# Kernel tuning notes

Hardware: AMD Instinct MI355X
Metric: run time of the kernel (lower is better)

The kernel has to match this reference:

```python
import jax, jax.numpy as jnp
import numpy as np

NUM_HEADS = 16
HEAD_DIM = 64  # d_out // num_heads


def setup_inputs() -> dict:
    key = jax.random.key(0)
    ks = jax.random.split(key, 6)
    d_in, d_out, b, t = 1024, 1024, 2, 2048
    s = 0.02
    return {
        "x": jax.random.normal(ks[0], (b, t, d_in), jnp.float32),
        "Wq": jax.random.normal(ks[1], (d_in, d_out), jnp.float32) * s,
        "Wk": jax.random.normal(ks[2], (d_in, d_out), jnp.float32) * s,
        "Wv": jax.random.normal(ks[3], (d_in, d_out), jnp.float32) * s,
        "Wo": jax.random.normal(ks[4], (d_out, d_out), jnp.float32) * s,
        "bo": jnp.zeros((d_out,), jnp.float32),
    }


def reference(x, Wq, Wk, Wv, Wo, bo):
    b, t, _ = x.shape
    H, hd = NUM_HEADS, HEAD_DIM
    # qkv projections (no bias), split into heads: [b, H, t, hd]
    q = (x @ Wq).reshape(b, t, H, hd).transpose(0, 2, 1, 3)
    k = (x @ Wk).reshape(b, t, H, hd).transpose(0, 2, 1, 3)
    v = (x @ Wv).reshape(b, t, H, hd).transpose(0, 2, 1, 3)
    # raw scores, causal mask (masked_fill with -1e9 BEFORE the 1/sqrt(hd) scale,
    # matching the source exactly), then scaled softmax
    scores = jnp.einsum("bhqd,bhkd->bhqk", q, k)
    causal = jnp.triu(jnp.ones((t, t), dtype=bool), k=1)
    scores = jnp.where(causal[None, None], jnp.float32(-1e9), scores)
    attn = jax.nn.softmax(scores / jnp.sqrt(jnp.float32(hd)), axis=-1)
    # dropout is identity in eval mode
    ctx = jnp.einsum("bhqk,bhkd->bhqd", attn, v)  # [b, H, t, hd]
    ctx = ctx.transpose(0, 2, 1, 3).reshape(b, t, H * hd)
    return ctx @ Wo + bo
```

## Files before the change

kernel.cpp:

```cpp
#include <hip/hip_runtime.h>


#define SEQ   2048
#define DMODEL 1024
#define NH    16
#define HD    64
#define MROWS 4096

typedef __attribute__((ext_vector_type(4))) float f32x4;
typedef __attribute__((ext_vector_type(16))) float f32x16;
typedef __attribute__((ext_vector_type(8))) short short8;
typedef __attribute__((ext_vector_type(4))) unsigned int u32x4;

#define MFMA16(a, b, c) __builtin_amdgcn_mfma_f32_16x16x32_bf16((a), (b), (c), 0, 0, 0)
#define MFMA32(a, b, c) __builtin_amdgcn_mfma_f32_32x32x16_bf16((a), (b), (c), 0, 0, 0)

__device__ __forceinline__ unsigned short f2bf(float f) {
  union { float f; unsigned u; } v; v.f = f;
  return (unsigned short)((v.u + 0x7fffu + ((v.u >> 16) & 1u)) >> 16);
}

__device__ __forceinline__ float exp2x(float x) {
#if __has_builtin(__builtin_amdgcn_exp2f)
  return __builtin_amdgcn_exp2f(x);
#else
  float r; asm("v_exp_f32 %0, %1" : "=v"(r) : "v"(x)); return r;
#endif
}

__device__ __forceinline__ unsigned cvt_pk(float lo, float hi) {
  unsigned r;
  asm volatile("v_cvt_pk_bf16_f32 %0, %1, %2" : "=v"(r) : "v"(lo), "v"(hi));
  return r;
}

__device__ __forceinline__ void pls(unsigned& a, unsigned& b) {
  asm("v_permlane32_swap_b32 %0, %1" : "+v"(a), "+v"(b));
}

__device__ __forceinline__ short8 as_short8(u32x4 v) {
  union { u32x4 u; short8 s; } x; x.u = v; return x.s;
}

__device__ __forceinline__ f32x4 zero4() {
  f32x4 z; z[0] = 0.f; z[1] = 0.f; z[2] = 0.f; z[3] = 0.f; return z;
}

__device__ __forceinline__ void async16(const void* g, void* l) {
  __builtin_amdgcn_global_load_lds(
      (const __attribute__((address_space(1))) unsigned int*)g,
      (__attribute__((address_space(3))) unsigned int*)l, 16, 0, 0);
}

__global__ __launch_bounds__(256) void xconv(const float* __restrict__ x,
                                             unsigned short* __restrict__ xb) {
  int i = blockIdx.x * 256 + threadIdx.x;
  const float4* p = (const float4*)x;
  float4 a = p[2 * i];
  float4 b = p[2 * i + 1];
  short8 o;
  o[0] = (short)f2bf(a.x); o[1] = (short)f2bf(a.y);
  o[2] = (short)f2bf(a.z); o[3] = (short)f2bf(a.w);
  o[4] = (short)f2bf(b.x); o[5] = (short)f2bf(b.y);
  o[6] = (short)f2bf(b.z); o[7] = (short)f2bf(b.w);
  *(short8*)&xb[(size_t)i * 8] = o;
}

__global__ __launch_bounds__(256) void wtrans(const float* __restrict__ W,
                                              unsigned short* __restrict__ Wt) {
  __shared__ unsigned short tile[64][65];
  int t = threadIdx.x;
  int tx = t & 63, ty = t >> 6;
  int kb = blockIdx.x * 64, nb = blockIdx.y * 64;
#pragma unroll
  for (int rr = 0; rr < 16; rr++) {
    int r = ty * 16 + rr;
    tile[r][tx] = f2bf(W[(size_t)(kb + r) * 1024 + nb + tx]);
  }
  __syncthreads();
#pragma unroll
  for (int rr = 0; rr < 16; rr++) {
    int r = ty * 16 + rr;
    Wt[(size_t)(nb + r) * 1024 + kb + tx] = tile[tx][r];
  }
}

__global__ __launch_bounds__(256) void vtrans(const unsigned short* __restrict__ V,
                                              unsigned short* __restrict__ Vt) {
  __shared__ unsigned short tile[64][65];
  int t = threadIdx.x;
  int tx = t & 63, ty = t >> 6;
  int bh = blockIdx.x, t0 = blockIdx.y * 64;
  const unsigned short* src = V + ((size_t)bh * SEQ + t0) * HD;
  unsigned short* dst = Vt + (size_t)bh * HD * SEQ + t0;
#pragma unroll
  for (int rr = 0; rr < 16; rr++) {
    int r = ty * 16 + rr;
    tile[r][tx] = src[(size_t)r * HD + tx];
  }
  __syncthreads();
#pragma unroll
  for (int rr = 0; rr < 16; rr++) {
    int r = ty * 16 + rr;
    dst[(size_t)r * SEQ + tx] = tile[tx][r];
  }
}

template <int MODE, int WMF>
__global__ __launch_bounds__(256) void gemm_bt(
    const unsigned short* __restrict__ A, const unsigned short* __restrict__ Bt,
    unsigned short* __restrict__ Qo, unsigned short* __restrict__ Ko,
    unsigned short* __restrict__ Vo, float* __restrict__ out,
    const float* __restrict__ bo) {
  constexpr int K = 1024;
  constexpr int BM = WMF * 32;
  constexpr int NT = K / 32;
  __shared__ __align__(16) unsigned short As[3][BM * 32];
  __shared__ __align__(16) unsigned short Bs[3][128 * 32];
  const int t = threadIdx.x;
  const int lane = t & 63;
  const int w = t >> 6;
  const int lr = lane & 15, kf = lane >> 4;
  const int wr = w >> 1, wc = w & 1;

  const int nwg = gridDim.x * gridDim.y;
  const int id = blockIdx.y * gridDim.x + blockIdx.x;
  const int swz = (id & 7) * (nwg >> 3) + (id >> 3);
  const int bx = swz % gridDim.x, by = swz / gridDim.x;

  const int rowbase = bx * BM;
  const int colbase = by * 128;

  const unsigned short* Ab = A + (size_t)rowbase * K;
  const unsigned short* Bb = Bt + (size_t)colbase * K;

  f32x4 acc[WMF][4];
#pragma unroll
  for (int m = 0; m < WMF; m++)
#pragma unroll
    for (int n = 0; n < 4; n++) acc[m][n] = zero4();

  auto stage = [&](int buf, int kt) {
    int k0 = kt * 32;
#pragma unroll
    for (int i = 0; i < BM / 64; i++) {
      int f = i * 256 + t;
      int c = f ^ ((f >> 3) & 3);
      int row = c >> 2;
      int col = (c & 3) << 3;
      async16(Ab + (size_t)row * K + k0 + col, (char*)&As[buf][0] + (size_t)f * 16);
    }
#pragma unroll
    for (int i = 0; i < 2; i++) {
      int f = i * 256 + t;
      int c = f ^ ((f >> 3) & 3);
      int row = c >> 2;
      int col = (c & 3) << 3;
      async16(Bb + (size_t)row * K + k0 + col, (char*)&Bs[buf][0] + (size_t)f * 16);
    }
  };

  stage(0, 0);
  stage(1, 1);

  for (int kt = 0; kt < NT; kt++) {
    if (kt + 2 < NT) {
      stage((kt + 2) % 3, kt + 2);
      if constexpr (MODE == 0) asm volatile("s_waitcnt vmcnt(8)" ::: "memory");
      else                     asm volatile("s_waitcnt vmcnt(6)" ::: "memory");
    } else if (kt + 1 < NT) {
      if constexpr (MODE == 0) asm volatile("s_waitcnt vmcnt(4)" ::: "memory");
      else                     asm volatile("s_waitcnt vmcnt(3)" ::: "memory");
    } else {
      asm volatile("s_waitcnt vmcnt(0)" ::: "memory");
    }
    __builtin_amdgcn_s_barrier();

    const int cur = kt % 3;
    short8 av[WMF], bv[4];
#pragma unroll
    for (int m = 0; m < WMF; m++) {
      int row = wr * (WMF * 16) + m * 16 + lr;
      int idx = (row * 32 + kf * 8) ^ (((row >> 1) & 3) << 3);
      av[m] = *(const short8*)&As[cur][idx];
    }
#pragma unroll
    for (int n = 0; n < 4; n++) {
      int row = wc * 64 + n * 16 + lr;
      int idx = (row * 32 + kf * 8) ^ (((row >> 1) & 3) << 3);
      bv[n] = *(const short8*)&Bs[cur][idx];
    }
    __builtin_amdgcn_s_setprio(1);
#pragma unroll
    for (int m = 0; m < WMF; m++)
#pragma unroll
      for (int n = 0; n < 4; n++) acc[m][n] = MFMA16(av[m], bv[n], acc[m][n]);
    __builtin_amdgcn_s_setprio(0);
    __builtin_amdgcn_s_barrier();
  }

  if constexpr (MODE == 0) {
#pragma unroll
    for (int n = 0; n < 4; n++) {
      int c = colbase + wc * 64 + n * 16 + lr;
      int sel = c >> 10;
      int hh = (c >> 6) & 15;
      int dd = c & 63;
      unsigned short* dst = (sel == 0) ? Qo : ((sel == 1) ? Ko : Vo);
      const float sc = (sel == 0) ? 0.18033688011112042f : 1.0f;
#pragma unroll
      for (int m = 0; m < WMF; m++) {
        int r0 = rowbase + wr * (WMF * 16) + m * 16 + kf * 4;
#pragma unroll
        for (int i = 0; i < 4; i++) {
          int r = r0 + i;
          int bi = r >> 11;
          int tq = r & 2047;
          size_t off = ((size_t)(bi * NH + hh) * SEQ + tq) * HD + dd;
          dst[off] = f2bf(acc[m][n][i] * sc);
        }
      }
    }
  } else {
#pragma unroll
    for (int n = 0; n < 4; n++) {
      int c = colbase + wc * 64 + n * 16 + lr;
      float bias = bo[c];
#pragma unroll
      for (int m = 0; m < WMF; m++) {
        int r0 = rowbase + wr * (WMF * 16) + m * 16 + kf * 4;
#pragma unroll
        for (int i = 0; i < 4; i++) {
          out[(size_t)(r0 + i) * 1024 + c] = acc[m][n][i] + bias;
        }
      }
    }
  }
}

__global__ __launch_bounds__(256) void attn_fwd(
    const unsigned short* __restrict__ Q, const unsigned short* __restrict__ K,
    const unsigned short* __restrict__ Vt, unsigned short* __restrict__ ctx) {
  const int bh = blockIdx.x;
  const int y = blockIdx.y;
  const int qt = (y < 8) ? (15 - y) : (y - 8);
  const int bi = bh >> 4, hh = bh & 15;
  const int t = threadIdx.x, lane = t & 63, w = t >> 6;
  const int qc = lane & 31, hi = lane >> 5;

  __shared__ __align__(16) unsigned short Ks[2][2][64 * 64];
  __shared__ __align__(16) unsigned short Vs[2][2][64 * 64];

  const unsigned short* Qb = Q + (size_t)bh * SEQ * HD;
  const unsigned short* Kb = K + (size_t)bh * SEQ * HD;
  const unsigned short* Vb = Vt + (size_t)bh * HD * SEQ;

  const int qrow = qt * 128 + w * 32;
  short8 qv[4];
#pragma unroll
  for (int c = 0; c < 4; c++)
    qv[c] = *(const short8*)&Qb[(size_t)(qrow + qc) * HD + c * 16 + hi * 8];

  f32x16 o0, o1;
#pragma unroll
  for (int i = 0; i < 16; i++) { o0[i] = 0.f; o1[i] = 0.f; }
  float l_acc = 0.f;

  const int ktmax = 2 * qt + (w >> 1);
  const int NP = qt + 1;

  auto stage = [&](int buf, int p) {
#pragma unroll
    for (int sub = 0; sub < 2; sub++) {
      int kt = 2 * p + sub;
#pragma unroll
      for (int i2 = 0; i2 < 2; i2++) {
        int f = i2 * 256 + t;
        int c = f ^ ((f >> 3) & 7);
        async16(Kb + (size_t)kt * 64 * HD + (size_t)c * 8,
                (char*)&Ks[buf][sub][0] + (size_t)f * 16);
        int d = c >> 3, ko = (c & 7) << 3;
        async16(Vb + (size_t)d * SEQ + (size_t)kt * 64 + ko,
                (char*)&Vs[buf][sub][0] + (size_t)f * 16);
      }
    }
  };

  auto tile = [&](const unsigned short* Kt, const unsigned short* Vtile, int kt) {
    f32x16 s0, s1;
#pragma unroll
    for (int i = 0; i < 16; i++) { s0[i] = 0.f; s1[i] = 0.f; }
    __builtin_amdgcn_s_setprio(1);
#pragma unroll
    for (int c = 0; c < 4; c++) {
      int i0 = (qc * 64 + c * 16 + hi * 8) ^ ((qc & 7) << 3);
      s0 = MFMA32(*(const short8*)&Kt[i0], qv[c], s0);
      int r1 = 32 + qc;
      int i1 = (r1 * 64 + c * 16 + hi * 8) ^ ((r1 & 7) << 3);
      s1 = MFMA32(*(const short8*)&Kt[i1], qv[c], s1);
    }
    __builtin_amdgcn_s_setprio(0);

    if (kt == ktmax) {
      const int qg = qrow + qc;
#pragma unroll
      for (int reg = 0; reg < 16; reg++) {
        int rloc = (reg & 3) + 8 * (reg >> 2) + 4 * hi;
        int kg = kt * 64 + rloc;
        if (kg > qg) s0[reg] = -1e30f;
        if (kg + 32 > qg) s1[reg] = -1e30f;
      }
    }

    unsigned w0[8], w1[8];
    float psA = 0.f, psB = 0.f;
#pragma unroll
    for (int j = 0; j < 8; j++) {
      float a0 = exp2x(s0[2 * j]), b0 = exp2x(s0[2 * j + 1]);
      float a1 = exp2x(s1[2 * j]), b1 = exp2x(s1[2 * j + 1]);
      psA += a0 + b0;
      psB += a1 + b1;
      w0[j] = cvt_pk(a0, b0);
      w1[j] = cvt_pk(a1, b1);
    }
    l_acc += psA + psB;

    __builtin_amdgcn_s_setprio(1);
#pragma unroll
    for (int h2 = 0; h2 < 2; h2++) {
      unsigned* pw = h2 ? w1 : w0;
#pragma unroll
      for (int cc = 0; cc < 2; cc++) {
        unsigned a0 = pw[cc * 4 + 0], b0 = pw[cc * 4 + 2];
        unsigned a1 = pw[cc * 4 + 1], b1 = pw[cc * 4 + 3];
        pls(a0, b0);
        pls(a1, b1);
        u32x4 pf; pf[0] = a0; pf[1] = a1; pf[2] = b0; pf[3] = b1;
        short8 pfrag = as_short8(pf);
        int c2 = h2 * 2 + cc;
        int ia = (qc * 64 + c2 * 16 + hi * 8) ^ ((qc & 7) << 3);
        o0 = MFMA32(*(const short8*)&Vtile[ia], pfrag, o0);
        int rb = 32 + qc;
        int ib = (rb * 64 + c2 * 16 + hi * 8) ^ ((rb & 7) << 3);
        o1 = MFMA32(*(const short8*)&Vtile[ib], pfrag, o1);
      }
    }
    __builtin_amdgcn_s_setprio(0);
  };

  stage(0, 0);
  int cur = 0;

  for (int p = 0; p < NP; p++) {
    if (p + 1 < NP) {
      stage(cur ^ 1, p + 1);
      asm volatile("s_waitcnt vmcnt(8)" ::: "memory");
    } else {
      asm volatile("s_waitcnt vmcnt(0)" ::: "memory");
    }
    __builtin_amdgcn_s_barrier();

    if (2 * p <= ktmax)     tile(&Ks[cur][0][0], &Vs[cur][0][0], 2 * p);
    if (2 * p + 1 <= ktmax) tile(&Ks[cur][1][0], &Vs[cur][1][0], 2 * p + 1);

    __builtin_amdgcn_s_barrier();
    cur ^= 1;
  }

  float l = l_acc + __shfl_xor(l_acc, 32);
  float inv = 1.0f / l;
  const size_t rowoff = ((size_t)bi * SEQ + qrow + qc) * DMODEL + hh * HD;
#pragma unroll
  for (int g = 0; g < 4; g++) {
    unsigned pa = cvt_pk(o0[4 * g] * inv, o0[4 * g + 1] * inv);
    unsigned pb = cvt_pk(o0[4 * g + 2] * inv, o0[4 * g + 3] * inv);
    uint2 vv; vv.x = pa; vv.y = pb;
    *(uint2*)&ctx[rowoff + 8 * g + 4 * hi] = vv;
    unsigned pc = cvt_pk(o1[4 * g] * inv, o1[4 * g + 1] * inv);
    unsigned pd = cvt_pk(o1[4 * g + 2] * inv, o1[4 * g + 3] * inv);
    uint2 ww; ww.x = pc; ww.y = pd;
    *(uint2*)&ctx[rowoff + 32 + 8 * g + 4 * hi] = ww;
  }
}

extern "C" void kernel_launch(void* const* d_in, const int* in_sizes, int n_in,
                              void* d_out, int out_size, void* d_ws, size_t ws_size,
                              hipStream_t stream) {
  const float* x  = (const float*)d_in[0];
  const float* Wq = (const float*)d_in[1];
  const float* Wk = (const float*)d_in[2];
  const float* Wv = (const float*)d_in[3];
  const float* Wo = (const float*)d_in[4];
  const float* bo = (const float*)d_in[5];
  float* out = (float*)d_out;

  unsigned short* xb   = (unsigned short*)d_ws;
  unsigned short* Wt   = xb + (size_t)MROWS * DMODEL;
  unsigned short* WoT  = Wt + (size_t)3 * 1024 * 1024;
  unsigned short* Qb   = WoT + (size_t)1024 * 1024;
  unsigned short* Kb   = Qb + (size_t)MROWS * DMODEL;
  unsigned short* Vb   = Kb + (size_t)MROWS * DMODEL;
  unsigned short* ctxb = Vb + (size_t)MROWS * DMODEL;

  xconv<<<2048, 256, 0, stream>>>(x, xb);
  dim3 tg(16, 16);
  wtrans<<<tg, 256, 0, stream>>>(Wq, Wt);
  wtrans<<<tg, 256, 0, stream>>>(Wk, Wt + (size_t)1024 * 1024);
  wtrans<<<tg, 256, 0, stream>>>(Wv, Wt + (size_t)2 * 1024 * 1024);
  wtrans<<<tg, 256, 0, stream>>>(Wo, WoT);

  gemm_bt<0, 4><<<dim3(32, 24), 256, 0, stream>>>(xb, Wt, Qb, Kb, ctxb, nullptr, nullptr);
  vtrans<<<dim3(32, 32), 256, 0, stream>>>(ctxb, Vb);
  attn_fwd<<<dim3(32, 16), 256, 0, stream>>>(Qb, Kb, Vb, ctxb);
  gemm_bt<1, 2><<<dim3(64, 8), 256, 0, stream>>>(ctxb, WoT, nullptr, nullptr, nullptr, out, bo);
}
```

Measured before the change: 121.1 us.

## Merge input conversion kernels into one prep launch and single-tile attention pipeline

After: 120.8 us. Within noise of the previous version (-0.2%).

```diff
diff --git a/kernel.cpp b/kernel.cpp
--- a/kernel.cpp
+++ b/kernel.cpp
@@ -52,26 +52,34 @@
       (__attribute__((address_space(3))) unsigned int*)l, 16, 0, 0);
 }
 
-__global__ __launch_bounds__(256) void xconv(const float* __restrict__ x,
-                                             unsigned short* __restrict__ xb) {
-  int i = blockIdx.x * 256 + threadIdx.x;
-  const float4* p = (const float4*)x;
-  float4 a = p[2 * i];
-  float4 b = p[2 * i + 1];
-  short8 o;
-  o[0] = (short)f2bf(a.x); o[1] = (short)f2bf(a.y);
-  o[2] = (short)f2bf(a.z); o[3] = (short)f2bf(a.w);
-  o[4] = (short)f2bf(b.x); o[5] = (short)f2bf(b.y);
-  o[6] = (short)f2bf(b.z); o[7] = (short)f2bf(b.w);
-  *(short8*)&xb[(size_t)i * 8] = o;
-}
-
-__global__ __launch_bounds__(256) void wtrans(const float* __restrict__ W,
-                                              unsigned short* __restrict__ Wt) {
+__global__ __launch_bounds__(256) void prep(
+    const float* __restrict__ x, const float* __restrict__ Wq,
+    const float* __restrict__ Wk, const float* __restrict__ Wv,
+    const float* __restrict__ Wo, unsigned short* __restrict__ xb,
+    unsigned short* __restrict__ Wt, unsigned short* __restrict__ WoT) {
   __shared__ unsigned short tile[64][65];
-  int t = threadIdx.x;
-  int tx = t & 63, ty = t >> 6;
-  int kb = blockIdx.x * 64, nb = blockIdx.y * 64;
+  const int bx = blockIdx.x;
+  if (bx < 2048) {
+    int i = bx * 256 + threadIdx.x;
+    const float4* p = (const float4*)x;
+    float4 a = p[2 * i];
+    float4 b = p[2 * i + 1];
+    short8 o;
+    o[0] = (short)f2bf(a.x); o[1] = (short)f2bf(a.y);
+    o[2] = (short)f2bf(a.z); o[3] = (short)f2bf(a.w);
+    o[4] = (short)f2bf(b.x); o[5] = (short)f2bf(b.y);
+    o[6] = (short)f2bf(b.z); o[7] = (short)f2bf(b.w);
+    *(short8*)&xb[(size_t)i * 8] = o;
+    return;
+  }
+  const int id2 = bx - 2048;
+  const int m = id2 >> 8;
+  const float* W = (m == 0) ? Wq : (m == 1) ? Wk : (m == 2) ? Wv : Wo;
+  unsigned short* D = (m == 3) ? WoT : Wt + (size_t)m * 1024 * 1024;
+  const int tid = id2 & 255;
+  const int kb = (tid >> 4) * 64, nb = (tid & 15) * 64;
+  const int t = threadIdx.x;
+  const int tx = t & 63, ty = t >> 6;
 #pragma unroll
   for (int rr = 0; rr < 16; rr++) {
     int r = ty * 16 + rr;
@@ -81,7 +89,7 @@
 #pragma unroll
   for (int rr = 0; rr < 16; rr++) {
     int r = ty * 16 + rr;
-    Wt[(size_t)(nb + r) * 1024 + kb + tx] = tile[tx][r];
+    D[(size_t)(nb + r) * 1024 + kb + tx] = tile[tx][r];
   }
 }
 
@@ -248,8 +256,8 @@
   const int t = threadIdx.x, lane = t & 63, w = t >> 6;
   const int qc = lane & 31, hi = lane >> 5;
 
-  __shared__ __align__(16) unsigned short Ks[2][2][64 * 64];
-  __shared__ __align__(16) unsigned short Vs[2][2][64 * 64];
+  __shared__ __align__(16) unsigned short Ks[2][64 * 64];
+  __shared__ __align__(16) unsigned short Vs[2][64 * 64];
 
   const unsigned short* Qb = Q + (size_t)bh * SEQ * HD;
   const unsigned short* Kb = K + (size_t)bh * SEQ * HD;
@@ -267,22 +275,18 @@
   float l_acc = 0.f;
 
   const int ktmax = 2 * qt + (w >> 1);
-  const int NP = qt + 1;
-
-  auto stage = [&](int buf, int p) {
-#pragma unroll
-    for (int sub = 0; sub < 2; sub++) {
-      int kt = 2 * p + sub;
-#pragma unroll
-      for (int i2 = 0; i2 < 2; i2++) {
-        int f = i2 * 256 + t;
-        int c = f ^ ((f >> 3) & 7);
-        async16(Kb + (size_t)kt * 64 * HD + (size_t)c * 8,
-                (char*)&Ks[buf][sub][0] + (size_t)f * 16);
-        int d = c >> 3, ko = (c & 7) << 3;
-        async16(Vb + (size_t)d * SEQ + (size_t)kt * 64 + ko,
-                (char*)&Vs[buf][sub][0] + (size_t)f * 16);
-      }
+  const int KT = 2 * qt + 2;
+
+  auto stage = [&](int buf, int kt) {
+#pragma unroll
+    for (int i2 = 0; i2 < 2; i2++) {
+      int f = i2 * 256 + t;
+      int c = f ^ ((f >> 3) & 7);
+      async16(Kb + (size_t)kt * 64 * HD + (size_t)c * 8,
+              (char*)&Ks[buf][0] + (size_t)f * 16);
+      int d = c >> 3, ko = (c & 7) << 3;
+      async16(Vb + (size_t)d * SEQ + (size_t)kt * 64 + ko,
+              (char*)&Vs[buf][0] + (size_t)f * 16);
     }
   };
 
@@ -351,17 +355,16 @@
   stage(0, 0);
   int cur = 0;
 
-  for (int p = 0; p < NP; p++) {
-    if (p + 1 < NP) {
-      stage(cur ^ 1, p + 1);
-      asm volatile("s_waitcnt vmcnt(8)" ::: "memory");
+  for (int kt = 0; kt < KT; kt++) {
+    if (kt + 1 < KT) {
+      stage(cur ^ 1, kt + 1);
+      asm volatile("s_waitcnt vmcnt(4)" ::: "memory");
     } else {
       asm volatile("s_waitcnt vmcnt(0)" ::: "memory");
     }
     __builtin_amdgcn_s_barrier();
 
-    if (2 * p <= ktmax)     tile(&Ks[cur][0][0], &Vs[cur][0][0], 2 * p);
-    if (2 * p + 1 <= ktmax) tile(&Ks[cur][1][0], &Vs[cur][1][0], 2 * p + 1);
+    if (kt <= ktmax) tile(&Ks[cur][0], &Vs[cur][0], kt);
 
     __builtin_amdgcn_s_barrier();
     cur ^= 1;
@@ -402,12 +405,7 @@
   unsigned short* Vb   = Kb + (size_t)MROWS * DMODEL;
   unsigned short* ctxb = Vb + (size_t)MROWS * DMODEL;
 
-  xconv<<<2048, 256, 0, stream>>>(x, xb);
-  dim3 tg(16, 16);
-  wtrans<<<tg, 256, 0, stream>>>(Wq, Wt);
-  wtrans<<<tg, 256, 0, stream>>>(Wk, Wt + (size_t)1024 * 1024);
-  wtrans<<<tg, 256, 0, stream>>>(Wv, Wt + (size_t)2 * 1024 * 1024);
-  wtrans<<<tg, 256, 0, stream>>>(Wo, WoT);
+  prep<<<3072, 256, 0, stream>>>(x, Wq, Wk, Wv, Wo, xb, Wt, WoT);
 
   gemm_bt<0, 4><<<dim3(32, 24), 256, 0, stream>>>(xb, Wt, Qb, Kb, ctxb, nullptr, nullptr);
   vtrans<<<dim3(32, 32), 256, 0, stream>>>(ctxb, Vb);
```
